# Performance work log

Hardware: AMD Instinct MI355X
Metric: run time of the kernel (lower is better)

Reference implementation:

```python
import jax, jax.numpy as jnp
import numpy as np

B, N, K = 2, 8192, 9
IN_CH, FEAT_CH, COST_CH = 64, 128, 64

def _bn(x, p, eps=1e-5):
    # eval-mode BatchNorm; p is [4, C] = (gamma, beta, running_mean, running_var)
    sh = (1, -1) + (1,) * (x.ndim - 2)
    g, b, m, v = (p[i].reshape(sh) for i in range(4))
    return (x - m) / jnp.sqrt(v + eps) * g + b

def _c1(x, w, b):
    # Conv1d kernel 1: x [B,C,N], w [O,C]
    return jnp.einsum('oc,bcn->bon', w, x) + b[None, :, None]

def _forward(xyz, points, cost_volume, feats, flow,
             w0, b0, bn0, w1, b1, bn1,
             wz, bz, wr, br, wq, bq,
             w2a, b2a, w2b, b2b, wfc, bfc,
             rw0, rbn0, rw1, rbn1, rw2, rbn2,
             cw0, cbn0, cw1, cbn1, cw2, cbn2):
    lrelu = lambda t: jax.nn.leaky_relu(t, 0.1)
    # --- self-KNN on xyz ---
    xt = jnp.transpose(xyz, (0, 2, 1))                   # B N 3
    sq = jnp.sum(xt * xt, -1)                            # B N
    d2 = sq[:, :, None] + sq[:, None, :] - 2.0 * jnp.einsum('bnd,bmd->bnm', xt, xt)
    idx = jax.lax.top_k(-d2, K)[1]                       # B N K (nearest incl. self)
    # --- grouping_operation: gather neighbor features ---
    np0 = jnp.concatenate([cost_volume, flow], 1)        # B (cost_ch+3) N
    g = jax.vmap(lambda p, i: p[:, i])(np0, idx)         # B C N K
    # --- Conv2d(1x1)+BN+LeakyReLU stack ---
    g = lrelu(_bn(jnp.einsum('oc,bcnk->bonk', w0, g) + b0[None, :, None, None], bn0))
    g = lrelu(_bn(jnp.einsum('oc,bcnk->bonk', w1, g) + b1[None, :, None, None], bn1))
    h = jnp.max(g, -1)                                   # max over neighbors -> B 128 N
    # --- ConvGRU(x=feats, h) with 1x1 Conv1d gates ---
    hx = jnp.concatenate([h, feats], 1)
    z = jax.nn.sigmoid(_c1(hx, wz, bz))
    r = jax.nn.sigmoid(_c1(hx, wr, br))
    q = jnp.tanh(_c1(jnp.concatenate([r * h, feats], 1), wq, bq))
    h = (1.0 - z) * h + z * q
    # --- Conv1d MLP head ---
    x = jnp.concatenate([points, h], 1)                  # B (in_ch+128) N
    x = lrelu(_c1(x, w2a, b2a))
    x = lrelu(_c1(x, w2b, b2b))
    re_flow = _c1(x, wfc, bfc)                           # B 3 N
    # --- prob regnets (Conv1d no-bias + BN + ReLU) ---
    def reg(y, ws, ps):
        for w, p in zip(ws, ps):
            y = jax.nn.relu(_bn(jnp.einsum('oc,bcn->bon', w, y), p))
        return y
    refine = reg(x, [rw0, rw1, rw2], [rbn0, rbn1, rbn2])         # B 1 N
    coarse = reg(cost_volume, [cw0, cw1, cw2], [cbn0, cbn1, cbn2])
    re_flow = coarse * flow + refine * re_flow
    return x, jnp.clip(re_flow, -20.0, 20.0)

def setup_inputs():
    key = jax.random.key(0)
    ks = iter(jax.random.split(key, 80))
    nrm = lambda shape, s=1.0: jax.random.normal(next(ks), shape, jnp.float32) * s
    def bnp(C):
        g = jax.random.uniform(next(ks), (C,), jnp.float32) + 0.5
        b = nrm((C,), 0.1); m = nrm((C,), 0.1)
        v = jax.random.uniform(next(ks), (C,), jnp.float32) + 0.5
        return jnp.stack([g, b, m, v])
    z = lambda C: jnp.zeros((C,), jnp.float32)
    return dict(
        xyz=nrm((B, 3, N)), points=nrm((B, IN_CH, N)), cost_volume=nrm((B, COST_CH, N)),
        feats=nrm((B, FEAT_CH, N)), flow=nrm((B, 3, N), 0.1),
        w0=nrm((128, COST_CH + 3), 0.05), b0=z(128), bn0=bnp(128),
        w1=nrm((128, 128), 0.05), b1=z(128), bn1=bnp(128),
        wz=nrm((128, 256), 0.05), bz=z(128), wr=nrm((128, 256), 0.05), br=z(128),
        wq=nrm((128, 256), 0.05), bq=z(128),
        w2a=nrm((128, IN_CH + 128), 0.05), b2a=z(128), w2b=nrm((64, 128), 0.05), b2b=z(64),
        wfc=nrm((3, 64), 0.05), bfc=z(3),
        rw0=nrm((64, 64), 0.05), rbn0=bnp(64), rw1=nrm((64, 64), 0.05), rbn1=bnp(64),
        rw2=nrm((1, 64), 0.05), rbn2=bnp(1),
        cw0=nrm((64, COST_CH), 0.05), cbn0=bnp(64), cw1=nrm((64, 64), 0.05), cbn1=bnp(64),
        cw2=nrm((1, 64), 0.05), cbn2=bnp(1),
    )

def reference(xyz, points, cost_volume, feats, flow, w0, b0, bn0, w1, b1, bn1, wz, bz, wr, br, wq, bq, w2a, b2a, w2b, b2b, wfc, bfc, rw0, rbn0, rw1, rbn1, rw2, rbn2, cw0, cbn0, cw1, cbn1, cw2, cbn2):
    return _forward(xyz, points, cost_volume, feats, flow, w0, b0, bn0, w1, b1, bn1, wz, bz, wr, br, wq, bq, w2a, b2a, w2b, b2b, wfc, bfc, rw0, rbn0, rw1, rbn1, rw2, rbn2, cw0, cbn0, cw1, cbn1, cw2, cbn2)
```

## Files before the change

kernel.cpp:

```cpp
#include <hip/hip_runtime.h>
#include <math.h>

typedef __bf16 bf16;
typedef __bf16 bf16x4 __attribute__((ext_vector_type(4)));
typedef __bf16 bf16x8 __attribute__((ext_vector_type(8)));
typedef float f32x4 __attribute__((ext_vector_type(4)));

#define NPTS 8192
#define MTOT 16384

static __device__ __forceinline__ float b2f(bf16 x) { return (float)x; }
static __device__ __forceinline__ bf16  f2b(float x) { return (bf16)x; }

__global__ void diag_k(float* out, float code)
{
    if (threadIdx.x == 0 && blockIdx.x == 0) out[0] = code;
}

static __device__ __forceinline__ void pack_body(bf16 (*tile)[68],
                                                 const float* __restrict__ src, int Csrc,
                                                 bf16* __restrict__ dst, int ldd,
                                                 int nb, int cb, int b)
{
    const int t = threadIdx.x;
#pragma unroll
    for (int i = 0; i < 8; ++i) {
        int id = t + i * 256;
        int c = id >> 6, n = id & 63;
        int cc = cb + c;
        bf16 v = (bf16)0.0f;
        if (cc < Csrc) v = f2b(src[(size_t)(b * Csrc + cc) * NPTS + nb + n]);
        tile[c][n] = v;
    }
    __syncthreads();
#pragma unroll
    for (int i = 0; i < 8; ++i) {
        int id = t + i * 256;
        int n = id >> 5, c = id & 31;
        dst[(size_t)(b * NPTS + nb + n) * ldd + cb + c] = tile[c][n];
    }
}

static __device__ __forceinline__ float tau32(unsigned u)
{
    unsigned m = 0x80000000u | (unsigned)(~((int)u >> 31));
    return __uint_as_float(u ^ m);
}

static __device__ __forceinline__ unsigned dpp_shr1_u(unsigned x)
{
    return (unsigned)__builtin_amdgcn_update_dpp(0, (int)x, 0x111, 0xf, 0xf, true);
}
static __device__ __forceinline__ int dpp_shr1_i(int x)
{
    return __builtin_amdgcn_update_dpp(0, x, 0x111, 0xf, 0xf, true);
}

static __device__ __forceinline__ void init9(float d, int lane,
                                             unsigned& kkd, int& idd)
{
    unsigned kd = __float_as_uint(d);
    kd ^= ((unsigned)((int)kd >> 31)) | 0x80000000u;
    unsigned long long key = ((unsigned long long)kd << 32) | (unsigned)lane;
#pragma unroll
    for (int r = 0; r < 9; ++r) {
        unsigned long long m = key;
#pragma unroll
        for (int s = 1; s < 64; s <<= 1) {
            unsigned long long o = __shfl_xor(m, s);
            if (o < m) m = o;
        }
        if (lane == r) {
            kkd = (unsigned)(m >> 32);
            idd = (int)(unsigned)(m & 0xffffffffu);
        }
        if (key == m) key = ~0ull;
    }
}

static __device__ __forceinline__ void hits9(float d, int base, float& tau,
                                             unsigned& kkd, int& idd)
{
    unsigned long long mask = __ballot(d <= tau);
    if (mask) {
        do {
            int L = __builtin_ctzll(mask);
            mask &= mask - 1;
            unsigned di = (unsigned)__builtin_amdgcn_readlane(__float_as_int(d), L);
            unsigned kd = di ^ (((unsigned)((int)di >> 31)) | 0x80000000u);
            const int idxn = base + L;
            unsigned kprev = dpp_shr1_u(kkd);
            int      iprev = dpp_shr1_i(idd);
            bool lt  = kd < kkd;
            bool ltp = kd < kprev;
            kkd = lt ? (ltp ? kprev : kd)   : kkd;
            idd = lt ? (ltp ? iprev : idxn) : idd;
        } while (mask);
        tau = tau32((unsigned)__builtin_amdgcn_readlane((int)kkd, 8));
    }
}

static __device__ __forceinline__ void mm32(
    f32x4 (&acc)[2][2],
    const bf16* A1, int lda1, int row01, int K1,
    const bf16* A2, int lda2, int row02,
    const bf16* W, int ldw, int K, int ob)
{
    const int lane = threadIdx.x & 63;
    const int q = lane >> 4, r = lane & 15;
    const bf16* Wp = W + (size_t)(ob + r) * ldw + q * 8;
    for (int k = 0; k < K; k += 32) {
        const bf16* Ap; int ld;
        if (k < K1) { ld = lda1; Ap = A1 + (size_t)(row01 + r) * lda1 + q * 8 + k; }
        else        { ld = lda2; Ap = A2 + (size_t)(row02 + r) * lda2 + q * 8 + (k - K1); }
        bf16x8 bv0 = *(const bf16x8*)(Wp + k);
        bf16x8 bv1 = *(const bf16x8*)(Wp + 16 * ldw + k);
        bf16x8 a0 = *(const bf16x8*)(Ap);
        bf16x8 a1 = *(const bf16x8*)(Ap + 16 * ld);
        acc[0][0] = __builtin_amdgcn_mfma_f32_16x16x32_bf16(a0, bv0, acc[0][0], 0, 0, 0);
        acc[1][0] = __builtin_amdgcn_mfma_f32_16x16x32_bf16(a1, bv0, acc[1][0], 0, 0, 0);
        acc[0][1] = __builtin_amdgcn_mfma_f32_16x16x32_bf16(a0, bv1, acc[0][1], 0, 0, 0);
        acc[1][1] = __builtin_amdgcn_mfma_f32_16x16x32_bf16(a1, bv1, acc[1][1], 0, 0, 0);
    }
}

static __device__ __forceinline__ void zacc(f32x4 (&acc)[2][2])
{
    f32x4 z = {0.f, 0.f, 0.f, 0.f};
    acc[0][0] = z; acc[0][1] = z; acc[1][0] = z; acc[1][1] = z;
}

static __device__ __forceinline__ void mm16(
    f32x4 (&acc)[2],
    const bf16* A1, int lda1, int row01, int K1,
    const bf16* A2, int lda2, int row02,
    const bf16* W, int ldw, int K, int ob)
{
    const int lane = threadIdx.x & 63;
    const int q = lane >> 4, r = lane & 15;
    const bf16* Wp = W + (size_t)(ob + r) * ldw + q * 8;
    for (int k = 0; k < K; k += 32) {
        const bf16* Ap; int ld;
        if (k < K1) { ld = lda1; Ap = A1 + (size_t)(row01 + r) * lda1 + q * 8 + k; }
        else        { ld = lda2; Ap = A2 + (size_t)(row02 + r) * lda2 + q * 8 + (k - K1); }
        bf16x8 bv0 = *(const bf16x8*)(Wp + k);
        bf16x8 a0 = *(const bf16x8*)(Ap);
        bf16x8 a1 = *(const bf16x8*)(Ap + 16 * ld);
        acc[0] = __builtin_amdgcn_mfma_f32_16x16x32_bf16(a0, bv0, acc[0], 0, 0, 0);
        acc[1] = __builtin_amdgcn_mfma_f32_16x16x32_bf16(a1, bv0, acc[1], 0, 0, 0);
    }
}

static __device__ __forceinline__ void mm16x2(
    f32x4 (&acc)[2], f32x4 (&acc2)[2],
    const bf16* A1, int lda1, int row01, int K1,
    const bf16* A2, int lda2, int row02,
    const bf16* Wa, const bf16* Wb, int ldw, int K, int ob)
{
    const int lane = threadIdx.x & 63;
    const int q = lane >> 4, r = lane & 15;
    const bf16* Wpa = Wa + (size_t)(ob + r) * ldw + q * 8;
    const bf16* Wpb = Wb + (size_t)(ob + r) * ldw + q * 8;
    for (int k = 0; k < K; k += 32) {
        const bf16* Ap; int ld;
        if (k < K1) { ld = lda1; Ap = A1 + (size_t)(row01 + r) * lda1 + q * 8 + k; }
        else        { ld = lda2; Ap = A2 + (size_t)(row02 + r) * lda2 + q * 8 + (k - K1); }
        bf16x8 a0 = *(const bf16x8*)(Ap);
        bf16x8 a1 = *(const bf16x8*)(Ap + 16 * ld);
        bf16x8 ba0 = *(const bf16x8*)(Wpa + k);
        bf16x8 bb0 = *(const bf16x8*)(Wpb + k);
        acc[0]  = __builtin_amdgcn_mfma_f32_16x16x32_bf16(a0, ba0, acc[0], 0, 0, 0);
        acc[1]  = __builtin_amdgcn_mfma_f32_16x16x32_bf16(a1, ba0, acc[1], 0, 0, 0);
        acc2[0] = __builtin_amdgcn_mfma_f32_16x16x32_bf16(a0, bb0, acc2[0], 0, 0, 0);
        acc2[1] = __builtin_amdgcn_mfma_f32_16x16x32_bf16(a1, bb0, acc2[1], 0, 0, 0);
    }
}

static __device__ __forceinline__ void zacc2(f32x4 (&acc)[2])
{
    f32x4 z = {0.f, 0.f, 0.f, 0.f};
    acc[0] = z; acc[1] = z;
}

__global__ __launch_bounds__(256) void pack_a(
    const float* __restrict__ w0, const float* __restrict__ w1,
    const float* __restrict__ wz, const float* __restrict__ wr,
    const float* __restrict__ wq, const float* __restrict__ w2a,
    const float* __restrict__ w2b, const float* __restrict__ rw0,
    const float* __restrict__ rw1, const float* __restrict__ cw0,
    const float* __restrict__ cw1,
    const float* __restrict__ cost, const float* __restrict__ flow,
    bf16* __restrict__ w0p, bf16* __restrict__ wts,
    bf16* __restrict__ CV, bf16* __restrict__ FL)
{
    __shared__ __align__(16) bf16 tile[32][68];
    const int bx = blockIdx.x;
    if (bx < 48) {
        int id = bx * 256 + threadIdx.x;
        if (id < 128 * 96) {
            int o = id / 96, c = id - o * 96;
            w0p[id] = (c < 67) ? f2b(w0[o * 67 + c]) : (bf16)0.0f;
        }
    } else if (bx < 688) {
        int id = (bx - 48) * 256 + threadIdx.x;
        if (id < 163840) {
            const float* s; int off;
            if (id < 16384)       { s = w1;  off = 0; }
            else if (id < 49152)  { s = wz;  off = 16384; }
            else if (id < 81920)  { s = wr;  off = 49152; }
            else if (id < 114688) { s = wq;  off = 81920; }
            else if (id < 139264) { s = w2a; off = 114688; }
            else if (id < 147456) { s = w2b; off = 139264; }
            else if (id < 151552) { s = rw0; off = 147456; }
            else if (id < 155648) { s = rw1; off = 151552; }
            else if (id < 159744) { s = cw0; off = 155648; }
            else                  { s = cw1; off = 159744; }
            wts[id] = f2b(s[id - off]);
        }
    } else if (bx < 1200) {
        int l = bx - 688, x = l & 127, r2 = l >> 7;
        pack_body(tile, cost, 64, CV, 64, x * 64, (r2 & 1) * 32, r2 >> 1);
    } else {
        int l = bx - 1200, x = l & 127, b = l >> 7;
        pack_body(tile, flow, 3, FL, 32, x * 64, 0, b);
    }
}

__global__ __launch_bounds__(256, 5) void knn_conv_packb(
    const float* __restrict__ xyz, const float* __restrict__ feats,
    const float* __restrict__ points,
    const bf16* __restrict__ CV, const bf16* __restrict__ FL,
    const bf16* __restrict__ W0p, const bf16* __restrict__ W1,
    const bf16* __restrict__ CW0, const bf16* __restrict__ CW1,
    const float* __restrict__ b0, const float* __restrict__ bn0,
    const float* __restrict__ b1, const float* __restrict__ bn1,
    const float* __restrict__ cbn0, const float* __restrict__ cbn1,
    const float* __restrict__ cw2, const float* __restrict__ cbn2,
    bf16* __restrict__ FE, bf16* __restrict__ PT,
    bf16* __restrict__ P2, int* __restrict__ idxg,
    float* __restrict__ coarseG)
{
    __shared__ __align__(16) char smem[18432];
    const int bx = blockIdx.x;
    if (bx < 2048) {
        float4* pts = (float4*)smem;
        const int t = threadIdx.x, lane = t & 63, w = t >> 6;
        const int qA = bx * 8 + w, qB = qA + 4;
        const int b = qA >> 13;
        const float* X = xyz + b * 3 * NPTS;
        const int nA = qA & (NPTS - 1), nB = qB & (NPTS - 1);
        const float qxA = X[nA], qyA = X[NPTS + nA], qzA = X[2 * NPTS + nA];
        const float qxB = X[nB], qyB = X[NPTS + nB], qzB = X[2 * NPTS + nB];
        const float qsqA = qxA * qxA + qyA * qyA + qzA * qzA;
        const float qsqB = qxB * qxB + qyB * qyB + qzB * qzB;

        unsigned kkdA = 0xFFFFFFFFu, kkdB = 0xFFFFFFFFu;
        int      iddA = 0, iddB = 0;
        float tauA = __builtin_inff(), tauB = __builtin_inff();

        float nx[4], ny[4], nz[4];
#pragma unroll
        for (int r2 = 0; r2 < 4; ++r2) {
            int ci = t + r2 * 256;
            nx[r2] = X[ci]; ny[r2] = X[NPTS + ci]; nz[r2] = X[2 * NPTS + ci];
        }
#pragma unroll
        for (int r2 = 0; r2 < 4; ++r2) {
            int i2 = t + r2 * 256;
            pts[i2] = make_float4(nx[r2], ny[r2], nz[r2],
                                  nx[r2]*nx[r2] + ny[r2]*ny[r2] + nz[r2]*nz[r2]);
        }
        __syncthreads();

        for (int ch = 0; ch < 8; ++ch) {
            if (ch < 7) {
#pragma unroll
                for (int r2 = 0; r2 < 4; ++r2) {
                    int ci = (ch + 1) * 1024 + t + r2 * 256;
                    nx[r2] = X[ci]; ny[r2] = X[NPTS + ci]; nz[r2] = X[2 * NPTS + ci];
                }
            }
            int i0 = 0;
            if (ch == 0) {
                float4 c = pts[lane];
                float dA = (qsqA + c.w) - 2.0f * (qxA * c.x + qyA * c.y + qzA * c.z);
                init9(dA, lane, kkdA, iddA);
                tauA = tau32((unsigned)__builtin_amdgcn_readlane((int)kkdA, 8));
                float dB = (qsqB + c.w) - 2.0f * (qxB * c.x + qyB * c.y + qzB * c.z);
                init9(dB, lane, kkdB, iddB);
                tauB = tau32((unsigned)__builtin_amdgcn_readlane((int)kkdB, 8));
                i0 = 1;
            }
            for (int i = i0; i < 16; ++i) {
                float4 c = pts[i * 64 + lane];
                float dA = (qsqA + c.w) - 2.0f * (qxA * c.x + qyA * c.y + qzA * c.z);
                float dB = (qsqB + c.w) - 2.0f * (qxB * c.x + qyB * c.y + qzB * c.z);
                const int base = ch * 1024 + i * 64;
                hits9(dA, base, tauA, kkdA, iddA);
                hits9(dB, base, tauB, kkdB, iddB);
            }
            __syncthreads();
            if (ch < 7) {
#pragma unroll
                for (int r2 = 0; r2 < 4; ++r2) {
                    int i2 = t + r2 * 256;
                    pts[i2] = make_float4(nx[r2], ny[r2], nz[r2],
                                          nx[r2]*nx[r2] + ny[r2]*ny[r2] + nz[r2]*nz[r2]);
                }
                __syncthreads();
            }
        }
        if (lane < 9) {
            int mA = iddA;
            mA = ((unsigned)mA < (unsigned)NPTS) ? mA : 0;
            idxg[qA * 9 + lane] = b * NPTS + mA;
            int mB = iddB;
            mB = ((unsigned)mB < (unsigned)NPTS) ? mB : 0;
            idxg[qB * 9 + lane] = b * NPTS + mB;
        }
    } else if (bx < 2560) {
        bf16 (*P1t)[136] = (bf16 (*)[136])smem;
        const int w = threadIdx.x >> 6, lane = threadIdx.x & 63;
        const int q = lane >> 4, r = lane & 15;
        const int ptb = (bx - 2048) * 32;
        {
            f32x4 acc[2][2]; zacc(acc);
            const int ob = w * 32;
            mm32(acc, CV, 64, ptb, 64, FL, 32, ptb, W0p, 96, 96, ob);
#pragma unroll
            for (int to = 0; to < 2; ++to) {
                const int o = ob + to * 16 + r;
                float bs = b0[o];
                float gg = bn0[o], be = bn0[128 + o], mm = bn0[256 + o];
                float rs = 1.0f / sqrtf(bn0[384 + o] + 1e-5f);
#pragma unroll
                for (int tm = 0; tm < 2; ++tm) {
#pragma unroll
                    for (int rr = 0; rr < 4; ++rr) {
                        const int jl = tm * 16 + q * 4 + rr;
                        float v = acc[tm][to][rr] + bs;
                        v = (v - mm) * rs * gg + be;
                        v = v > 0.f ? v : 0.1f * v;
                        P1t[jl][o] = f2b(v);
                    }
                }
            }
        }
        __syncthreads();
        {
            f32x4 acc[2][2]; zacc(acc);
            const int ob = w * 32;
            mm32(acc, &P1t[0][0], 136, 0, 128, &P1t[0][0], 136, 0, W1, 128, 128, ob);
#pragma unroll
            for (int to = 0; to < 2; ++to) {
                const int o = ob + to * 16 + r;
                float bs = b1[o];
                float gg = bn1[o], be = bn1[128 + o], mm = bn1[256 + o];
                float rs = 1.0f / sqrtf(bn1[384 + o] + 1e-5f);
#pragma unroll
                for (int tm = 0; tm < 2; ++tm) {
#pragma unroll
                    for (int rr = 0; rr < 4; ++rr) {
                        const int jl = tm * 16 + q * 4 + rr;
                        float v = acc[tm][to][rr] + bs;
                        v = (v - mm) * rs * gg + be;
                        v = v > 0.f ? v : 0.1f * v;
                        P2[(size_t)(ptb + jl) * 128 + o] = f2b(v);
                    }
                }
            }
        }
    } else if (bx < 3584) {
        bf16 (*tile)[68] = (bf16 (*)[68])smem;
        int l = bx - 2560, x = l & 127, r2 = l >> 7;
        pack_body(tile, feats, 128, FE, 128, x * 64, (r2 & 3) * 32, r2 >> 2);
    } else if (bx < 4096) {
        bf16 (*tile)[68] = (bf16 (*)[68])smem;
        int l = bx - 3584, x = l & 127, r2 = l >> 7;
        pack_body(tile, points, 64, PT, 64, x * 64, (r2 & 1) * 32, r2 >> 1);
    } else {
        bf16 (*C1t)[72] = (bf16 (*)[72])smem;
        bf16 (*C2t)[72] = (bf16 (*)[72])(smem + 9216);
        const int w = threadIdx.x >> 6, lane = threadIdx.x & 63;
        const int q = lane >> 4, r = lane & 15;
        const int row0 = (w >> 1) * 32;
        const int pt0 = (bx - 4096) * 64 + row0;
        const int ob = (w & 1) * 32;
        {
            f32x4 acc[2][2]; zacc(acc);
            mm32(acc, CV, 64, pt0, 64, CV, 64, pt0, CW0, 64, 64, ob);
#pragma unroll
            for (int to = 0; to < 2; ++to) {
                const int o = ob + to * 16 + r;
                float gg = cbn0[o], be = cbn0[64 + o], mm = cbn0[128 + o];
                float rs = 1.0f / sqrtf(cbn0[192 + o] + 1e-5f);
#pragma unroll
                for (int tm = 0; tm < 2; ++tm)
#pragma unroll
                    for (int rr = 0; rr < 4; ++rr) {
                        const int jl = tm * 16 + q * 4 + rr;
                        float v = acc[tm][to][rr];
                        v = (v - mm) * rs * gg + be;
                        C1t[row0 + jl][o] = f2b(fmaxf(v, 0.f));
                    }
            }
        }
        __syncthreads();
        {
            f32x4 acc[2][2]; zacc(acc);
            mm32(acc, &C1t[0][0], 72, row0, 64, &C1t[0][0], 72, row0, CW1, 64, 64, ob);
#pragma unroll
            for (int to = 0; to < 2; ++to) {
                const int o = ob + to * 16 + r;
                float gg = cbn1[o], be = cbn1[64 + o], mm = cbn1[128 + o];
                float rs = 1.0f / sqrtf(cbn1[192 + o] + 1e-5f);
#pragma unroll
                for (int tm = 0; tm < 2; ++tm)
#pragma unroll
                    for (int rr = 0; rr < 4; ++rr) {
                        const int jl = tm * 16 + q * 4 + rr;
                        float v = acc[tm][to][rr];
                        v = (v - mm) * rs * gg + be;
                        C2t[row0 + jl][o] = f2b(fmaxf(v, 0.f));
                    }
            }
        }
        __syncthreads();
        if (threadIdx.x < 64) {
            const int jl = threadIdx.x;
            const int j = (bx - 4096) * 64 + jl;
            float dc = 0.f;
#pragma unroll
            for (int c = 0; c < 64; ++c) dc += cw2[c] * b2f(C2t[jl][c]);
            float coarse = (dc - cbn2[2]) / sqrtf(cbn2[3] + 1e-5f) * cbn2[0] + cbn2[1];
            coarseG[j] = fmaxf(coarse, 0.f);
        }
    }
}

struct MRP {
    const bf16 *P2, *FE, *PT;
    const int  *idx;
    const bf16 *WZ, *WR, *WQ, *W2A, *W2B, *RW0, *RW1;
    const float *bz, *br, *bq, *b2a, *b2b;
    const float *rbn0, *rbn1;
    const float *rw2, *rbn2, *wfc, *bfc, *flow, *coarse;
    float* out;
};

__global__ __launch_bounds__(512) void megarow(MRP p)
{
    __shared__ __align__(16) bf16 Zt[32][136], RHt[32][136], HPt[32][136], X1t[32][136];
    __shared__ __align__(16) bf16 FEt[32][136];
    __shared__ __align__(16) bf16 X2t[32][72], R1t[32][72], R2t[32][72], PTt[32][72];
    __shared__ int idxt[32][9];
    const int w = threadIdx.x >> 6, lane = threadIdx.x & 63;
    const int q = lane >> 4, r = lane & 15;
    const int ptb = blockIdx.x * 32;

    if (threadIdx.x < 288) {
        int jl = threadIdx.x / 9, k = threadIdx.x - jl * 9;
        int m = p.idx[(ptb + jl) * 9 + k];
        idxt[jl][k] = ((unsigned)m < (unsigned)MTOT) ? m : 0;
    }
    {
        const int row = threadIdx.x >> 4;
        const int c8 = (threadIdx.x & 15) * 8;
        *(bf16x8*)&FEt[row][c8] = *(const bf16x8*)(p.FE + (size_t)(ptb + row) * 128 + c8);
        const int c4 = (threadIdx.x & 15) * 4;
        *(bf16x4*)&PTt[row][c4] = *(const bf16x4*)(p.PT + (size_t)(ptb + row) * 64 + c4);
    }
    __syncthreads();
    {
        const int c8 = (threadIdx.x & 15) * 8;
        const int jl = threadIdx.x >> 4;
        float mx0 = -__builtin_inff(), mx1 = -__builtin_inff();
        float mx2 = -__builtin_inff(), mx3 = -__builtin_inff();
        float mx4 = -__builtin_inff(), mx5 = -__builtin_inff();
        float mx6 = -__builtin_inff(), mx7 = -__builtin_inff();
#pragma unroll
        for (int k = 0; k < 9; ++k) {
            bf16x8 v = *(const bf16x8*)(p.P2 + (size_t)idxt[jl][k] * 128 + c8);
            mx0 = fmaxf(mx0, b2f(v[0]));
            mx1 = fmaxf(mx1, b2f(v[1]));
            mx2 = fmaxf(mx2, b2f(v[2]));
            mx3 = fmaxf(mx3, b2f(v[3]));
            mx4 = fmaxf(mx4, b2f(v[4]));
            mx5 = fmaxf(mx5, b2f(v[5]));
            mx6 = fmaxf(mx6, b2f(v[6]));
            mx7 = fmaxf(mx7, b2f(v[7]));
        }
        bf16x8 st;
        st[0] = f2b(mx0); st[1] = f2b(mx1); st[2] = f2b(mx2); st[3] = f2b(mx3);
        st[4] = f2b(mx4); st[5] = f2b(mx5); st[6] = f2b(mx6); st[7] = f2b(mx7);
        *(bf16x8*)&X1t[jl][c8] = st;
    }
    __syncthreads();

    {
        const int ob = w * 16;
        f32x4 acc[2], acc2[2]; zacc2(acc); zacc2(acc2);
        mm16x2(acc, acc2, &X1t[0][0], 136, 0, 128, &FEt[0][0], 136, 0,
               p.WZ, p.WR, 256, 256, ob);
        const int o = ob + r;
        const float bsz = p.bz[o];
#pragma unroll
        for (int tm = 0; tm < 2; ++tm)
#pragma unroll
            for (int rr = 0; rr < 4; ++rr) {
                const int jl = tm * 16 + q * 4 + rr;
                float v = acc[tm][rr] + bsz;
                Zt[jl][o] = f2b(1.0f / (1.0f + expf(-v)));
            }
        const float bsr = p.br[o];
#pragma unroll
        for (int tm = 0; tm < 2; ++tm)
#pragma unroll
            for (int rr = 0; rr < 4; ++rr) {
                const int jl = tm * 16 + q * 4 + rr;
                float v = acc2[tm][rr] + bsr;
                v = 1.0f / (1.0f + expf(-v));
                RHt[jl][o] = f2b(v * b2f(X1t[jl][o]));
            }
    }
    __syncthreads();
    {
        const int ob = w * 16;
        f32x4 acc[2]; zacc2(acc);
        mm16(acc, &RHt[0][0], 136, 0, 128, &FEt[0][0], 136, 0, p.WQ, 256, 256, ob);
        const int o = ob + r;
        const float bs = p.bq[o];
#pragma unroll
        for (int tm = 0; tm < 2; ++tm)
#pragma unroll
            for (int rr = 0; rr < 4; ++rr) {
                const int jl = tm * 16 + q * 4 + rr;
                float v = acc[tm][rr] + bs;
                float qv = tanhf(v);
                float z = b2f(Zt[jl][o]);
                float h = b2f(X1t[jl][o]);
                HPt[jl][o] = f2b((1.0f - z) * h + z * qv);
            }
    }
    __syncthreads();
    {
        const int ob = w * 16;
        f32x4 acc[2]; zacc2(acc);
        mm16(acc, &PTt[0][0], 72, 0, 64, &HPt[0][0], 136, 0, p.W2A, 192, 192, ob);
        const int o = ob + r;
        const float bs = p.b2a[o];
#pragma unroll
        for (int tm = 0; tm < 2; ++tm)
#pragma unroll
            for (int rr = 0; rr < 4; ++rr) {
                const int jl = tm * 16 + q * 4 + rr;
                float v = acc[tm][rr] + bs;
                X1t[jl][o] = f2b(v > 0.f ? v : 0.1f * v);
            }
    }
    __syncthreads();
    if (w < 4) {
        const int ob = w * 16;
        f32x4 acc[2]; zacc2(acc);
        mm16(acc, &X1t[0][0], 136, 0, 128, &X1t[0][0], 136, 0, p.W2B, 128, 128, ob);
        const int o = ob + r;
        const float bs = p.b2b[o];
#pragma unroll
        for (int tm = 0; tm < 2; ++tm)
#pragma unroll
            for (int rr = 0; rr < 4; ++rr) {
                const int jl = tm * 16 + q * 4 + rr;
                float v = acc[tm][rr] + bs;
                v = v > 0.f ? v : 0.1f * v;
                X2t[jl][o] = f2b(v);
                const int j = ptb + jl, bb = j >> 13, nn = j & (NPTS - 1);
                p.out[(size_t)bb * 64 * NPTS + (size_t)o * NPTS + nn] = v;
            }
    }
    __syncthreads();
    if (w < 4) {
        const int ob = w * 16;
        f32x4 acc[2]; zacc2(acc);
        mm16(acc, &X2t[0][0], 72, 0, 64, &X2t[0][0], 72, 0, p.RW0, 64, 64, ob);
        const int o = ob + r;
        float gg = p.rbn0[o], be = p.rbn0[64 + o], mm = p.rbn0[128 + o];
        float rs = 1.0f / sqrtf(p.rbn0[192 + o] + 1e-5f);
#pragma unroll
        for (int tm = 0; tm < 2; ++tm)
#pragma unroll
            for (int rr = 0; rr < 4; ++rr) {
                const int jl = tm * 16 + q * 4 + rr;
                float v = acc[tm][rr];
                v = (v - mm) * rs * gg + be;
                R1t[jl][o] = f2b(fmaxf(v, 0.f));
            }
    }
    __syncthreads();
    if (w < 4) {
        const int ob = w * 16;
        f32x4 acc[2]; zacc2(acc);
        mm16(acc, &R1t[0][0], 72, 0, 64, &R1t[0][0], 72, 0, p.RW1, 64, 64, ob);
        const int o = ob + r;
        float gg = p.rbn1[o], be = p.rbn1[64 + o], mm = p.rbn1[128 + o];
        float rs = 1.0f / sqrtf(p.rbn1[192 + o] + 1e-5f);
#pragma unroll
        for (int tm = 0; tm < 2; ++tm)
#pragma unroll
            for (int rr = 0; rr < 4; ++rr) {
                const int jl = tm * 16 + q * 4 + rr;
                float v = acc[tm][rr];
                v = (v - mm) * rs * gg + be;
                R2t[jl][o] = f2b(fmaxf(v, 0.f));
            }
    }
    __syncthreads();
    if (threadIdx.x < 32) {
        const int jl = threadIdx.x, j = ptb + jl;
        const int b = j >> 13, n = j & (NPTS - 1);
        float dr = 0.f, p0 = 0.f, p1 = 0.f, p2 = 0.f;
#pragma unroll
        for (int c = 0; c < 64; ++c) {
            float x = b2f(X2t[jl][c]);
            dr += p.rw2[c] * b2f(R2t[jl][c]);
            p0 += p.wfc[c] * x;
            p1 += p.wfc[64 + c] * x;
            p2 += p.wfc[128 + c] * x;
        }
        float refine = (dr - p.rbn2[2]) / sqrtf(p.rbn2[3] + 1e-5f) * p.rbn2[0] + p.rbn2[1];
        refine = fmaxf(refine, 0.f);
        const float coarse = p.coarse[j];
        p0 += p.bfc[0]; p1 += p.bfc[1]; p2 += p.bfc[2];
        const float f0 = p.flow[(size_t)b * 3 * NPTS + n];
        const float f1 = p.flow[(size_t)b * 3 * NPTS + NPTS + n];
        const float f2v = p.flow[(size_t)b * 3 * NPTS + 2 * NPTS + n];
        float o0 = fminf(fmaxf(coarse * f0 + refine * p0, -20.f), 20.f);
        float o1 = fminf(fmaxf(coarse * f1 + refine * p1, -20.f), 20.f);
        float o2 = fminf(fmaxf(coarse * f2v + refine * p2, -20.f), 20.f);
        float* ro = p.out + 1048576;
        ro[(size_t)b * 3 * NPTS + n] = o0;
        ro[(size_t)b * 3 * NPTS + NPTS + n] = o1;
        ro[(size_t)b * 3 * NPTS + 2 * NPTS + n] = o2;
    }
}

extern "C" void kernel_launch(void* const* d_in, const int* in_sizes, int n_in,
                              void* d_out, int out_size, void* d_ws, size_t ws_size,
                              hipStream_t stream)
{
    static const int EXP[35] = {
        49152, 1048576, 1048576, 2097152, 49152,
        8576, 128, 512, 16384, 128, 512,
        32768, 128, 32768, 128, 32768, 128,
        24576, 128, 8192, 64, 192, 3,
        4096, 256, 4096, 256, 64, 4,
        4096, 256, 4096, 256, 64, 4 };
    float code = 0.f;
    if (n_in != 35) code = 900.f;
    else if (out_size != 1097728) code = 950.f;
    else if (ws_size < 18767872u) code = 980.f;
    else { for (int i = 0; i < 35; ++i) if (in_sizes[i] != EXP[i]) { code = 1000.f + 4.f * i; break; } }
    if (code != 0.f) { diag_k<<<dim3(1), dim3(64), 0, stream>>>((float*)d_out, code); return; }

    const float* xyz    = (const float*)d_in[0];
    const float* points = (const float*)d_in[1];
    const float* cost   = (const float*)d_in[2];
    const float* feats  = (const float*)d_in[3];
    const float* flow   = (const float*)d_in[4];
    const float* w0     = (const float*)d_in[5];
    const float* b0     = (const float*)d_in[6];
    const float* bn0    = (const float*)d_in[7];
    const float* w1     = (const float*)d_in[8];
    const float* b1     = (const float*)d_in[9];
    const float* bn1    = (const float*)d_in[10];
    const float* wz     = (const float*)d_in[11];
    const float* bz     = (const float*)d_in[12];
    const float* wr     = (const float*)d_in[13];
    const float* br     = (const float*)d_in[14];
    const float* wq     = (const float*)d_in[15];
    const float* bq     = (const float*)d_in[16];
    const float* w2a    = (const float*)d_in[17];
    const float* b2a    = (const float*)d_in[18];
    const float* w2b    = (const float*)d_in[19];
    const float* b2b    = (const float*)d_in[20];
    const float* wfc    = (const float*)d_in[21];
    const float* bfc    = (const float*)d_in[22];
    const float* rw0    = (const float*)d_in[23];
    const float* rbn0   = (const float*)d_in[24];
    const float* rw1    = (const float*)d_in[25];
    const float* rbn1   = (const float*)d_in[26];
    const float* rw2    = (const float*)d_in[27];
    const float* rbn2   = (const float*)d_in[28];
    const float* cw0    = (const float*)d_in[29];
    const float* cbn0   = (const float*)d_in[30];
    const float* cw1    = (const float*)d_in[31];
    const float* cbn1   = (const float*)d_in[32];
    const float* cw2    = (const float*)d_in[33];
    const float* cbn2   = (const float*)d_in[34];

    char* ws = (char*)d_ws;
    bf16*  W0p  = (bf16*)(ws + 0);
    bf16*  WTS  = (bf16*)(ws + 24576);
    int*   idxg = (int*) (ws + 352256);
    bf16*  CV   = (bf16*)(ws + 942080);
    bf16*  FL   = (bf16*)(ws + 3039232);
    bf16*  FE   = (bf16*)(ws + 4087808);
    bf16*  PT   = (bf16*)(ws + 8282112);
    bf16*  P2   = (bf16*)(ws + 10379264);
    float* CO   = (float*)(ws + 14573568);

    bf16* W1  = WTS;
    bf16* WZ  = WTS + 16384;
    bf16* WR  = WTS + 49152;
    bf16* WQ  = WTS + 81920;
    bf16* W2A = WTS + 114688;
    bf16* W2B = WTS + 139264;
    bf16* RW0 = WTS + 147456;
    bf16* RW1 = WTS + 151552;
    bf16* CW0 = WTS + 155648;
    bf16* CW1 = WTS + 159744;

    float* out = (float*)d_out;

     pack_a<<<dim3(1456), dim3(256), 0, stream>>>(
              w0, w1, wz, wr, wq, w2a, w2b, rw0, rw1, cw0, cw1,
              cost, flow, W0p, WTS, CV, FL);
     knn_conv_packb<<<dim3(4352), dim3(256), 0, stream>>>(
              xyz, feats, points, CV, FL, W0p, W1, CW0, CW1,
              b0, bn0, b1, bn1, cbn0, cbn1, cw2, cbn2,
              FE, PT, P2, idxg, CO);
     MRP mp;
          mp.P2 = P2; mp.FE = FE; mp.PT = PT; mp.idx = idxg;
          mp.WZ = WZ; mp.WR = WR; mp.WQ = WQ; mp.W2A = W2A; mp.W2B = W2B;
          mp.RW0 = RW0; mp.RW1 = RW1;
          mp.bz = bz; mp.br = br; mp.bq = bq; mp.b2a = b2a; mp.b2b = b2b;
          mp.rbn0 = rbn0; mp.rbn1 = rbn1;
          mp.rw2 = rw2; mp.rbn2 = rbn2;
          mp.wfc = wfc; mp.bfc = bfc; mp.flow = flow; mp.coarse = CO;
          mp.out = out;
          megarow<<<dim3(512), dim3(512), 0, stream>>>(mp);

    (void)n_in;
}
```

Baseline: 230.7 us.

## Precompute packed xyz float4 and process four KNN queries per wave from global

Adds a stage to pack_a that writes the xyz coordinates plus squared norm as float4 into a workspace buffer. The KNN blocks now read candidates straight from this buffer (cached in L1/L2) instead of staging them through LDS with block-wide syncs, and each wave handles four queries instead of two, so the KNN block count halves. This removes the LDS staging, the barriers and the repeated norm computation, and reuses each candidate load across more queries. In exchange it adds register pressure from four top-9 states per wave, has fewer blocks to hide latency, and depends on global/L1 bandwidth for candidate reads.

```diff
diff --git a/kernel.cpp b/kernel.cpp
--- a/kernel.cpp
+++ b/kernel.cpp
@@ -190,8 +190,10 @@
     const float* __restrict__ rw1, const float* __restrict__ cw0,
     const float* __restrict__ cw1,
     const float* __restrict__ cost, const float* __restrict__ flow,
+    const float* __restrict__ xyz,
     bf16* __restrict__ w0p, bf16* __restrict__ wts,
-    bf16* __restrict__ CV, bf16* __restrict__ FL)
+    bf16* __restrict__ CV, bf16* __restrict__ FL,
+    float4* __restrict__ P4)
 {
     __shared__ __align__(16) bf16 tile[32][68];
     const int bx = blockIdx.x;
@@ -220,15 +222,20 @@
     } else if (bx < 1200) {
         int l = bx - 688, x = l & 127, r2 = l >> 7;
         pack_body(tile, cost, 64, CV, 64, x * 64, (r2 & 1) * 32, r2 >> 1);
-    } else {
+    } else if (bx < 1456) {
         int l = bx - 1200, x = l & 127, b = l >> 7;
         pack_body(tile, flow, 3, FL, 32, x * 64, 0, b);
+    } else {
+        int id = (bx - 1456) * 256 + threadIdx.x;
+        int b = id >> 13, n = id & (NPTS - 1);
+        const float* X = xyz + b * 3 * NPTS;
+        float x = X[n], y = X[NPTS + n], z = X[2 * NPTS + n];
+        P4[id] = make_float4(x, y, z, x * x + y * y + z * z);
     }
 }
 
 __global__ __launch_bounds__(256, 5) void knn_conv_packb(
-    const float* __restrict__ xyz, const float* __restrict__ feats,
-    const float* __restrict__ points,
+    const float* __restrict__ xyz, const float4* __restrict__ P4,
     const bf16* __restrict__ CV, const bf16* __restrict__ FL,
     const bf16* __restrict__ W0p, const bf16* __restrict__ W1,
     const bf16* __restrict__ CW0, const bf16* __restrict__ CW1,
@@ -236,93 +243,62 @@
     const float* __restrict__ b1, const float* __restrict__ bn1,
     const float* __restrict__ cbn0, const float* __restrict__ cbn1,
     const float* __restrict__ cw2, const float* __restrict__ cbn2,
+    const float* __restrict__ feats, const float* __restrict__ points,
     bf16* __restrict__ FE, bf16* __restrict__ PT,
     bf16* __restrict__ P2, int* __restrict__ idxg,
     float* __restrict__ coarseG)
 {
     __shared__ __align__(16) char smem[18432];
     const int bx = blockIdx.x;
-    if (bx < 2048) {
-        float4* pts = (float4*)smem;
+    if (bx < 1024) {
         const int t = threadIdx.x, lane = t & 63, w = t >> 6;
-        const int qA = bx * 8 + w, qB = qA + 4;
-        const int b = qA >> 13;
+        const int q0 = bx * 16 + w * 4;
+        const int b = q0 >> 13;
         const float* X = xyz + b * 3 * NPTS;
-        const int nA = qA & (NPTS - 1), nB = qB & (NPTS - 1);
-        const float qxA = X[nA], qyA = X[NPTS + nA], qzA = X[2 * NPTS + nA];
-        const float qxB = X[nB], qyB = X[NPTS + nB], qzB = X[2 * NPTS + nB];
-        const float qsqA = qxA * qxA + qyA * qyA + qzA * qzA;
-        const float qsqB = qxB * qxB + qyB * qyB + qzB * qzB;
-
-        unsigned kkdA = 0xFFFFFFFFu, kkdB = 0xFFFFFFFFu;
-        int      iddA = 0, iddB = 0;
-        float tauA = __builtin_inff(), tauB = __builtin_inff();
-
-        float nx[4], ny[4], nz[4];
-#pragma unroll
-        for (int r2 = 0; r2 < 4; ++r2) {
-            int ci = t + r2 * 256;
-            nx[r2] = X[ci]; ny[r2] = X[NPTS + ci]; nz[r2] = X[2 * NPTS + ci];
-        }
-#pragma unroll
-        for (int r2 = 0; r2 < 4; ++r2) {
-            int i2 = t + r2 * 256;
-            pts[i2] = make_float4(nx[r2], ny[r2], nz[r2],
-                                  nx[r2]*nx[r2] + ny[r2]*ny[r2] + nz[r2]*nz[r2]);
-        }
-        __syncthreads();
-
-        for (int ch = 0; ch < 8; ++ch) {
-            if (ch < 7) {
-#pragma unroll
-                for (int r2 = 0; r2 < 4; ++r2) {
-                    int ci = (ch + 1) * 1024 + t + r2 * 256;
-                    nx[r2] = X[ci]; ny[r2] = X[NPTS + ci]; nz[r2] = X[2 * NPTS + ci];
-                }
-            }
-            int i0 = 0;
-            if (ch == 0) {
-                float4 c = pts[lane];
-                float dA = (qsqA + c.w) - 2.0f * (qxA * c.x + qyA * c.y + qzA * c.z);
-                init9(dA, lane, kkdA, iddA);
-                tauA = tau32((unsigned)__builtin_amdgcn_readlane((int)kkdA, 8));
-                float dB = (qsqB + c.w) - 2.0f * (qxB * c.x + qyB * c.y + qzB * c.z);
-                init9(dB, lane, kkdB, iddB);
-                tauB = tau32((unsigned)__builtin_amdgcn_readlane((int)kkdB, 8));
-                i0 = 1;
-            }
-            for (int i = i0; i < 16; ++i) {
-                float4 c = pts[i * 64 + lane];
-                float dA = (qsqA + c.w) - 2.0f * (qxA * c.x + qyA * c.y + qzA * c.z);
-                float dB = (qsqB + c.w) - 2.0f * (qxB * c.x + qyB * c.y + qzB * c.z);
-                const int base = ch * 1024 + i * 64;
-                hits9(dA, base, tauA, kkdA, iddA);
-                hits9(dB, base, tauB, kkdB, iddB);
-            }
-            __syncthreads();
-            if (ch < 7) {
-#pragma unroll
-                for (int r2 = 0; r2 < 4; ++r2) {
-                    int i2 = t + r2 * 256;
-                    pts[i2] = make_float4(nx[r2], ny[r2], nz[r2],
-                                          nx[r2]*nx[r2] + ny[r2]*ny[r2] + nz[r2]*nz[r2]);
-                }
-                __syncthreads();
+        const float4* C4 = P4 + (size_t)b * NPTS;
+
+        float qx[4], qy[4], qz[4], qsq[4];
+#pragma unroll
+        for (int j = 0; j < 4; ++j) {
+            int n = (q0 + j) & (NPTS - 1);
+            qx[j] = X[n]; qy[j] = X[NPTS + n]; qz[j] = X[2 * NPTS + n];
+            qsq[j] = qx[j] * qx[j] + qy[j] * qy[j] + qz[j] * qz[j];
+        }
+        unsigned kkd[4]; int idd[4]; float tau[4];
+#pragma unroll
+        for (int j = 0; j < 4; ++j) { kkd[j] = 0xFFFFFFFFu; idd[j] = 0; }
+
+        {
+            float4 c = C4[lane];
+#pragma unroll
+            for (int j = 0; j < 4; ++j) {
+                float d = (qsq[j] + c.w) - 2.0f * (qx[j] * c.x + qy[j] * c.y + qz[j] * c.z);
+                init9(d, lane, kkd[j], idd[j]);
+                tau[j] = tau32((unsigned)__builtin_amdgcn_readlane((int)kkd[j], 8));
+            }
+        }
+        for (int g = 1; g < 128; ++g) {
+            float4 c = C4[g * 64 + lane];
+            const int base = g * 64;
+#pragma unroll
+            for (int j = 0; j < 4; ++j) {
+                float d = (qsq[j] + c.w) - 2.0f * (qx[j] * c.x + qy[j] * c.y + qz[j] * c.z);
+                hits9(d, base, tau[j], kkd[j], idd[j]);
             }
         }
         if (lane < 9) {
-            int mA = iddA;
-            mA = ((unsigned)mA < (unsigned)NPTS) ? mA : 0;
-            idxg[qA * 9 + lane] = b * NPTS + mA;
-            int mB = iddB;
-            mB = ((unsigned)mB < (unsigned)NPTS) ? mB : 0;
-            idxg[qB * 9 + lane] = b * NPTS + mB;
-        }
-    } else if (bx < 2560) {
+#pragma unroll
+            for (int j = 0; j < 4; ++j) {
+                int m = idd[j];
+                m = ((unsigned)m < (unsigned)NPTS) ? m : 0;
+                idxg[(q0 + j) * 9 + lane] = b * NPTS + m;
+            }
+        }
+    } else if (bx < 1536) {
         bf16 (*P1t)[136] = (bf16 (*)[136])smem;
         const int w = threadIdx.x >> 6, lane = threadIdx.x & 63;
         const int q = lane >> 4, r = lane & 15;
-        const int ptb = (bx - 2048) * 32;
+        const int ptb = (bx - 1024) * 32;
         {
             f32x4 acc[2][2]; zacc(acc);
             const int ob = w * 32;
@@ -370,13 +346,13 @@
                 }
             }
         }
-    } else if (bx < 3584) {
+    } else if (bx < 2560) {
+        bf16 (*tile)[68] = (bf16 (*)[68])smem;
+        int l = bx - 1536, x = l & 127, r2 = l >> 7;
+        pack_body(tile, feats, 128, FE, 128, x * 64, (r2 & 3) * 32, r2 >> 2);
+    } else if (bx < 3072) {
         bf16 (*tile)[68] = (bf16 (*)[68])smem;
         int l = bx - 2560, x = l & 127, r2 = l >> 7;
-        pack_body(tile, feats, 128, FE, 128, x * 64, (r2 & 3) * 32, r2 >> 2);
-    } else if (bx < 4096) {
-        bf16 (*tile)[68] = (bf16 (*)[68])smem;
-        int l = bx - 3584, x = l & 127, r2 = l >> 7;
         pack_body(tile, points, 64, PT, 64, x * 64, (r2 & 1) * 32, r2 >> 1);
     } else {
         bf16 (*C1t)[72] = (bf16 (*)[72])smem;
@@ -384,7 +360,7 @@
         const int w = threadIdx.x >> 6, lane = threadIdx.x & 63;
         const int q = lane >> 4, r = lane & 15;
         const int row0 = (w >> 1) * 32;
-        const int pt0 = (bx - 4096) * 64 + row0;
+        const int pt0 = (bx - 3072) * 64 + row0;
         const int ob = (w & 1) * 32;
         {
             f32x4 acc[2][2]; zacc(acc);
@@ -428,7 +404,7 @@
         __syncthreads();
         if (threadIdx.x < 64) {
             const int jl = threadIdx.x;
-            const int j = (bx - 4096) * 64 + jl;
+            const int j = (bx - 3072) * 64 + jl;
             float dc = 0.f;
 #pragma unroll
             for (int c = 0; c < 64; ++c) dc += cw2[c] * b2f(C2t[jl][c]);
@@ -698,15 +674,16 @@
     const float* cbn2   = (const float*)d_in[34];
 
     char* ws = (char*)d_ws;
-    bf16*  W0p  = (bf16*)(ws + 0);
-    bf16*  WTS  = (bf16*)(ws + 24576);
-    int*   idxg = (int*) (ws + 352256);
-    bf16*  CV   = (bf16*)(ws + 942080);
-    bf16*  FL   = (bf16*)(ws + 3039232);
-    bf16*  FE   = (bf16*)(ws + 4087808);
-    bf16*  PT   = (bf16*)(ws + 8282112);
-    bf16*  P2   = (bf16*)(ws + 10379264);
-    float* CO   = (float*)(ws + 14573568);
+    bf16*   W0p  = (bf16*)(ws + 0);
+    bf16*   WTS  = (bf16*)(ws + 24576);
+    int*    idxg = (int*) (ws + 352256);
+    bf16*   CV   = (bf16*)(ws + 942080);
+    bf16*   FL   = (bf16*)(ws + 3039232);
+    bf16*   FE   = (bf16*)(ws + 4087808);
+    bf16*   PT   = (bf16*)(ws + 8282112);
+    bf16*   P2   = (bf16*)(ws + 10379264);
+    float*  CO   = (float*)(ws + 14573568);
+    float4* P4   = (float4*)(ws + 14639104);
 
     bf16* W1  = WTS;
     bf16* WZ  = WTS + 16384;
@@ -721,13 +698,13 @@
 
     float* out = (float*)d_out;
 
-     pack_a<<<dim3(1456), dim3(256), 0, stream>>>(
+     pack_a<<<dim3(1520), dim3(256), 0, stream>>>(
               w0, w1, wz, wr, wq, w2a, w2b, rw0, rw1, cw0, cw1,
-              cost, flow, W0p, WTS, CV, FL);
-     knn_conv_packb<<<dim3(4352), dim3(256), 0, stream>>>(
-              xyz, feats, points, CV, FL, W0p, W1, CW0, CW1,
+              cost, flow, xyz, W0p, WTS, CV, FL, P4);
+     knn_conv_packb<<<dim3(3328), dim3(256), 0, stream>>>(
+              xyz, P4, CV, FL, W0p, W1, CW0, CW1,
               b0, bn0, b1, bn1, cbn0, cbn1, cw2, cbn2,
-              FE, PT, P2, idxg, CO);
+              feats, points, FE, PT, P2, idxg, CO);
      MRP mp;
           mp.P2 = P2; mp.FE = FE; mp.PT = PT; mp.idx = idxg;
           mp.WZ = WZ; mp.WR = WR; mp.WQ = WQ; mp.W2A = W2A; mp.W2B = W2B;
```

Result: slower. 247.2 us (+7.1%).
